# Performance work log

Measured on AMD Instinct MI355X. Metric: run time of the kernel, lower is better.

## Reference

```python
import jax, jax.numpy as jnp
import numpy as np

B, N, D = 2, 8192, 128
TEMP_MIN = 1e-4


def setup_inputs() -> dict:
    key = jax.random.key(0)
    k0, k1 = jax.random.split(key)
    feats0 = jax.random.normal(k0, (B, N, D), dtype=jnp.float32)
    feats1 = jax.random.normal(k1, (B, N, D), dtype=jnp.float32)
    temp = jnp.ones((), dtype=jnp.float32)  # nn.Parameter(temp_init=1.0)
    return {"feats0": feats0, "feats1": feats1, "temp": temp}


def reference(feats0, feats1, temp):
    x2 = jnp.sum(feats0 * feats0, axis=-1, keepdims=True)            # [B, N0, 1]
    y2 = jnp.sum(feats1 * feats1, axis=-1, keepdims=True)            # [B, N1, 1]
    dists = x2 - 2.0 * jnp.einsum('bnd,bmd->bnm', feats0, feats1)
    dists = dists + jnp.swapaxes(y2, -2, -1)                          # [B, N0, N1]

    t = jnp.maximum(temp * temp, TEMP_MIN)                            # get_temp()
    probs = jax.nn.softmax(-dists / t, axis=-1)                       # [B, N0, N1]

    idx = jnp.argmax(probs, axis=-1)                                  # [B, N0]
    asgn = jax.nn.one_hot(idx, probs.shape[-1], dtype=probs.dtype)    # hard one-hot
    # straight-through: value = one-hot, gradient = softmax gradient
    asgn_diff = asgn - jax.lax.stop_gradient(probs) + probs
    return asgn_diff, idx
```

## Files before the change

kernel.cpp:

```cpp
#include <hip/hip_runtime.h>
#include <hip/hip_fp16.h>
#include <cstdint>
#include <cstddef>

#define NPTS 8192
#define DDIM 128
#define BATCH 2
#define NROWS (BATCH * NPTS)
#define EPSGAP 1.0f
#define NCOLT 64
#define WCAP 512

typedef __attribute__((ext_vector_type(8))) _Float16 half8v;
typedef __attribute__((ext_vector_type(4))) float f32x4;

typedef __attribute__((address_space(3))) unsigned int as3_uint;
typedef const __attribute__((address_space(1))) unsigned int as1_uint;

__global__ void split_kernel(const float* __restrict__ f0, const float* __restrict__ f1,
                             unsigned short* __restrict__ Aext, unsigned short* __restrict__ Bext,
                             float* __restrict__ y2) {
    const unsigned half = gridDim.x >> 1;
    const bool isB = blockIdx.x >= half;
    const float* src = isB ? f1 : f0;
    unsigned short* dst = isB ? Bext : Aext;
    size_t t = (size_t)(blockIdx.x - (isB ? half : 0)) * 256 + threadIdx.x;
    size_t row = t >> 5;
    int kc = (int)(t & 31) * 4;
    float4 v = reinterpret_cast<const float4*>(src)[t];
    ushort4 h;
    h.x = __half_as_ushort(__float2half(v.x));
    h.y = __half_as_ushort(__float2half(v.y));
    h.z = __half_as_ushort(__float2half(v.z));
    h.w = __half_as_ushort(__float2half(v.w));
    *reinterpret_cast<ushort4*>(&dst[row * 128 + kc]) = h;

    if (isB) {
        float s = fmaf(v.x, v.x, fmaf(v.y, v.y, fmaf(v.z, v.z, v.w * v.w)));
#pragma unroll
        for (int off = 16; off >= 1; off >>= 1) s += __shfl_xor(s, off);
        if ((t & 31) == 0) y2[row] = s;
    }
}

__global__ __launch_bounds__(256) void gemm_mfma(
    const unsigned short* __restrict__ Aext,
    const unsigned short* __restrict__ Bext,
    const float* __restrict__ y2g,
    float* __restrict__ pv1, float* __restrict__ pv2, unsigned int* __restrict__ pidx,
    float* __restrict__ outZero)
{
    __shared__ __align__(16) short As[128 * 64];
    __shared__ __align__(16) short Bs[128 * 64];
    __shared__ float rv1[2][128];
    __shared__ float rv2[2][128];
    __shared__ unsigned int ri[2][128];

    const unsigned flat = blockIdx.x;
    const unsigned wg   = (flat & 7u) * 1024u + (flat >> 3);
    const int bm  = wg & 63;
    const int bnc = (int)((wg >> 6) & 63);
    const int b   = (int)(wg >> 12);

    const int tid  = threadIdx.x;
    const int lane = tid & 63;
    const int wid  = tid >> 6;
    const int wr   = wid >> 1, wc = wid & 1;
    const int l15  = lane & 15, l4 = lane >> 4;
    const int row0 = bm * 128, col0 = bnc * 128;

    const unsigned short* Abase = Aext + ((size_t)b * NPTS + row0) * 128;
    const unsigned short* Bbase = Bext + ((size_t)b * NPTS + col0) * 128;

    f32x4 acc[4][4];
#pragma unroll
    for (int i = 0; i < 4; ++i)
#pragma unroll
        for (int j = 0; j < 4; ++j) acc[i][j] = (f32x4)0.0f;

#pragma unroll
    for (int kk = 0; kk < 2; ++kk) {
        __syncthreads();
        {
            const int ko = kk * 64;
#pragma unroll
            for (int it = 0; it < 4; ++it) {
                int flat2 = it * 256 + tid;
                int r = flat2 >> 3, kc = flat2 & 7;
                int kcs = kc ^ (r & 7);
                const unsigned short* ga = Abase + (size_t)r * 128 + ko + kcs * 8;
                const unsigned short* gb = Bbase + (size_t)r * 128 + ko + kcs * 8;
                __builtin_amdgcn_global_load_lds((as1_uint*)ga, (as3_uint*)&As[flat2 * 8], 16, 0, 0);
                __builtin_amdgcn_global_load_lds((as1_uint*)gb, (as3_uint*)&Bs[flat2 * 8], 16, 0, 0);
            }
        }
        __syncthreads();
#pragma unroll
        for (int ks = 0; ks < 2; ++ks) {
            half8v a[4], bf[4];
#pragma unroll
            for (int i = 0; i < 4; ++i) {
                int ra = wr * 64 + i * 16 + l15;
                int ch = ks * 4 + l4;
                a[i] = *reinterpret_cast<const half8v*>(&As[ra * 64 + ((ch ^ (ra & 7)) << 3)]);
            }
#pragma unroll
            for (int j = 0; j < 4; ++j) {
                int rb = wc * 64 + j * 16 + l15;
                int ch = ks * 4 + l4;
                bf[j] = *reinterpret_cast<const half8v*>(&Bs[rb * 64 + ((ch ^ (rb & 7)) << 3)]);
            }
#pragma unroll
            for (int i = 0; i < 4; ++i)
#pragma unroll
                for (int j = 0; j < 4; ++j)
                    acc[i][j] = __builtin_amdgcn_mfma_f32_16x16x32_f16(a[i], bf[j], acc[i][j], 0, 0, 0);
        }
    }

    const float* y2b = y2g + b * NPTS;
    float yv[4];
#pragma unroll
    for (int j = 0; j < 4; ++j) yv[j] = y2b[col0 + wc * 64 + j * 16 + l15];

    {
        f32x4* o4 = reinterpret_cast<f32x4*>(outZero) + (size_t)wg * 4096;
        const f32x4 z = (f32x4)0.0f;
#pragma unroll
        for (int it = 0; it < 16; ++it)
            __builtin_nontemporal_store(z, &o4[it * 256 + tid]);
    }

#pragma unroll
    for (int i = 0; i < 4; ++i) {
#pragma unroll
        for (int q = 0; q < 4; ++q) {
            float v1 = INFINITY, v2 = INFINITY;
            unsigned int mi = 0u;
#pragma unroll
            for (int j = 0; j < 4; ++j) {
                const float v = fmaf(-2.0f, acc[i][j][q], yv[j]);
                const unsigned int m = (unsigned)(col0 + wc * 64 + j * 16 + l15);
                if (v < v1) { v2 = v1; v1 = v; mi = m; }
                else        { v2 = fminf(v2, v); }
            }
#pragma unroll
            for (int off = 1; off < 16; off <<= 1) {
                float o1 = __shfl_xor(v1, off);
                float o2 = __shfl_xor(v2, off);
                unsigned int oi = __shfl_xor(mi, off);
                if (o1 < v1 || (o1 == v1 && oi < mi)) { v2 = fminf(v1, o2); v1 = o1; mi = oi; }
                else                                  { v2 = fminf(v2, fminf(o1, o2)); }
            }
            if (l15 == 0) {
                const int rl = wr * 64 + i * 16 + l4 * 4 + q;
                rv1[wc][rl] = v1; rv2[wc][rl] = v2; ri[wc][rl] = mi;
            }
        }
    }
    __syncthreads();
    if (tid < 128) {
        float a1 = rv1[0][tid], a2 = rv2[0][tid];
        unsigned int ai = ri[0][tid];
        const float o1 = rv1[1][tid], o2 = rv2[1][tid];
        const unsigned int oi = ri[1][tid];
        if (o1 < a1 || (o1 == a1 && oi < ai)) { a2 = fminf(a1, o2); a1 = o1; ai = oi; }
        else                                  { a2 = fminf(a2, fminf(o1, o2)); }
        const size_t gr = (size_t)b * NPTS + row0 + tid;
        pv1[(size_t)bnc * NROWS + gr] = a1;
        pv2[(size_t)bnc * NROWS + gr] = a2;
        pidx[(size_t)bnc * NROWS + gr] = ai;
    }
}

__global__ __launch_bounds__(256) void finalize_kernel(
    const float* __restrict__ f0, const float* __restrict__ f1,
    const float* __restrict__ pv1, const float* __restrict__ pv2,
    const unsigned int* __restrict__ pidx,
    float* __restrict__ out)
{
    __shared__ float xrow[4][DDIM];
    __shared__ unsigned int cand[4][WCAP];
    __shared__ int ncand[4];
    __shared__ float s_best[64];
    __shared__ unsigned char s_flag[64];
    __shared__ int s_nflag;

    const int tid = threadIdx.x;
    const int gr0 = blockIdx.x * 64;

    if (tid == 0) s_nflag = 0;
    __syncthreads();

    {
        const int r  = tid >> 2;
        const int q  = tid & 3;
        const int gr = gr0 + r;
        float a1 = INFINITY, a2 = INFINITY;
        unsigned int ai = 0u;
#pragma unroll 4
        for (int c = 0; c < 16; ++c) {
            const int cs = q * 16 + c;
            const size_t base = (size_t)cs * NROWS + gr;
            const float o1 = pv1[base];
            const float o2 = pv2[base];
            const unsigned int oi = pidx[base];
            if (o1 < a1 || (o1 == a1 && oi < ai)) { a2 = fminf(a1, o2); a1 = o1; ai = oi; }
            else                                  { a2 = fminf(a2, fminf(o1, o2)); }
        }
#pragma unroll
        for (int off = 1; off < 4; off <<= 1) {
            const float o1 = __shfl_xor(a1, off);
            const float o2 = __shfl_xor(a2, off);
            const unsigned int oi = __shfl_xor(ai, off);
            if (o1 < a1 || (o1 == a1 && oi < ai)) { a2 = fminf(a1, o2); a1 = o1; ai = oi; }
            else                                  { a2 = fminf(a2, fminf(o1, o2)); }
        }
        if (q == 0) {
            if (a2 - a1 < EPSGAP) {
                const int p = atomicAdd(&s_nflag, 1);
                s_flag[p] = (unsigned char)r;
                s_best[r] = a1;
            } else {
                out[(size_t)gr * NPTS + ai] = 1.0f;
                out[(size_t)BATCH * NPTS * NPTS + gr] = (float)ai;
            }
        }
    }
    __syncthreads();

    const int nf   = s_nflag;
    const int w    = tid >> 6;
    const int lane = tid & 63;

    for (int li = w; li < nf; li += 4) {
        const int rr = (int)s_flag[li];
        const int gr = gr0 + rr;
        const int b = gr >> 13, n = gr & (NPTS - 1);
        const float W = s_best[rr] + EPSGAP;

        if (lane == 0) ncand[w] = 0;
        const float* xp = f0 + ((size_t)b * NPTS + n) * DDIM;
        xrow[w][lane]      = xp[lane];
        xrow[w][lane + 64] = xp[lane + 64];

        {
            const size_t base = (size_t)lane * NROWS + gr;
            const float t1 = pv1[base];
            if (t1 <= W) {
                if (pv2[base] <= W) {
                    int p = atomicAdd(&ncand[w], 128);
                    if (p + 128 <= WCAP)
                        for (int c = 0; c < 128; ++c) cand[w][p + c] = (unsigned)(lane * 128 + c);
                } else {
                    int p = atomicAdd(&ncand[w], 1);
                    if (p < WCAP) cand[w][p] = pidx[base];
                }
            }
        }
        asm volatile("s_waitcnt lgkmcnt(0)" ::: "memory");

        const int nc = ncand[w];
        double bv = 1e300;
        unsigned int bi = 0xFFFFFFFFu;
        const float4* xpv = reinterpret_cast<const float4*>(xrow[w]);
        if (nc <= WCAP) {
            for (int c = lane; c < nc; c += 64) {
                const unsigned int m = cand[w][c];
                const float4* ypv = reinterpret_cast<const float4*>(f1 + ((size_t)b * NPTS + m) * DDIM);
                double s0 = 0.0, s1 = 0.0, s2 = 0.0, s3 = 0.0;
#pragma unroll 8
                for (int k4 = 0; k4 < DDIM / 4; ++k4) {
                    const float4 y = ypv[k4];
                    const float4 x = xpv[k4];
                    s0 = fma((double)y.x, (double)y.x - 2.0 * (double)x.x, s0);
                    s1 = fma((double)y.y, (double)y.y - 2.0 * (double)x.y, s1);
                    s2 = fma((double)y.z, (double)y.z - 2.0 * (double)x.z, s2);
                    s3 = fma((double)y.w, (double)y.w - 2.0 * (double)x.w, s3);
                }
                const double v = (s0 + s1) + (s2 + s3);
                if (v < bv || (v == bv && m < bi)) { bv = v; bi = m; }
            }
        } else {
            for (int m = lane; m < NPTS; m += 64) {
                const float4* ypv = reinterpret_cast<const float4*>(f1 + ((size_t)b * NPTS + m) * DDIM);
                double s0 = 0.0, s1 = 0.0, s2 = 0.0, s3 = 0.0;
#pragma unroll 4
                for (int k4 = 0; k4 < DDIM / 4; ++k4) {
                    const float4 y = ypv[k4];
                    const float4 x = xpv[k4];
                    s0 = fma((double)y.x, (double)y.x - 2.0 * (double)x.x, s0);
                    s1 = fma((double)y.y, (double)y.y - 2.0 * (double)x.y, s1);
                    s2 = fma((double)y.z, (double)y.z - 2.0 * (double)x.z, s2);
                    s3 = fma((double)y.w, (double)y.w - 2.0 * (double)x.w, s3);
                }
                const double v = (s0 + s1) + (s2 + s3);
                if (v < bv || (v == bv && (unsigned)m < bi)) { bv = v; bi = (unsigned)m; }
            }
        }
#pragma unroll
        for (int off = 1; off < 64; off <<= 1) {
            const double ov = __shfl_xor(bv, off);
            const unsigned int oi = __shfl_xor(bi, off);
            if (ov < bv || (ov == bv && oi < bi)) { bv = ov; bi = oi; }
        }
        if (lane == 0) {
            out[(size_t)gr * NPTS + bi] = 1.0f;
            out[(size_t)BATCH * NPTS * NPTS + gr] = (float)bi;
        }
        asm volatile("s_waitcnt lgkmcnt(0)" ::: "memory");
    }
}

extern "C" void kernel_launch(void* const* d_in, const int* in_sizes, int n_in,
                              void* d_out, int out_size, void* d_ws, size_t ws_size,
                              hipStream_t stream)
{
    const float* f0 = (const float*)d_in[0];
    const float* f1 = (const float*)d_in[1];
    float* out = (float*)d_out;

    char* wsb = (char*)d_ws;
    unsigned short* Aext = (unsigned short*)wsb;                  wsb += (size_t)BATCH * NPTS * 128 * 2;
    unsigned short* Bext = (unsigned short*)wsb;                  wsb += (size_t)BATCH * NPTS * 128 * 2;
    float* y2            = (float*)wsb;                           wsb += (size_t)NROWS * 4;
    float* pv1           = (float*)wsb;                           wsb += (size_t)NCOLT * NROWS * 4;
    float* pv2           = (float*)wsb;                           wsb += (size_t)NCOLT * NROWS * 4;
    unsigned int* pidx   = (unsigned int*)wsb;

    split_kernel<<<2 * (BATCH * NPTS * 32) / 256, 256, 0, stream>>>(f0, f1, Aext, Bext, y2);
    gemm_mfma<<<NPTS / 128 * NPTS / 128 * BATCH, 256, 0, stream>>>(Aext, Bext, y2, pv1, pv2, pidx, out);
    finalize_kernel<<<NROWS / 64, 256, 0, stream>>>(f0, f1, pv1, pv2, pidx, out);
}
```

Baseline: 193.5 us.

## Fuse fp16 conversion and column norms into GEMM, drop split kernel

Removes the separate split kernel that converted features to fp16 and computed y2. The GEMM now loads fp32 tiles straight into LDS in four 32-wide phases and converts to fp16 in registers with cvt_pkrtz. It also accumulates the B-row squared norms from the same LDS reads and reduces them through shared memory. The block-to-XCD mapping is changed as well. This saves a launch and the intermediate global round trip, at the cost of twice the global and LDS traffic per tile, more barriers, and round-toward-zero conversion.

```diff
diff --git a/kernel.cpp b/kernel.cpp
--- a/kernel.cpp
+++ b/kernel.cpp
@@ -17,50 +17,33 @@
 typedef __attribute__((address_space(3))) unsigned int as3_uint;
 typedef const __attribute__((address_space(1))) unsigned int as1_uint;
 
-__global__ void split_kernel(const float* __restrict__ f0, const float* __restrict__ f1,
-                             unsigned short* __restrict__ Aext, unsigned short* __restrict__ Bext,
-                             float* __restrict__ y2) {
-    const unsigned half = gridDim.x >> 1;
-    const bool isB = blockIdx.x >= half;
-    const float* src = isB ? f1 : f0;
-    unsigned short* dst = isB ? Bext : Aext;
-    size_t t = (size_t)(blockIdx.x - (isB ? half : 0)) * 256 + threadIdx.x;
-    size_t row = t >> 5;
-    int kc = (int)(t & 31) * 4;
-    float4 v = reinterpret_cast<const float4*>(src)[t];
-    ushort4 h;
-    h.x = __half_as_ushort(__float2half(v.x));
-    h.y = __half_as_ushort(__float2half(v.y));
-    h.z = __half_as_ushort(__float2half(v.z));
-    h.w = __half_as_ushort(__float2half(v.w));
-    *reinterpret_cast<ushort4*>(&dst[row * 128 + kc]) = h;
-
-    if (isB) {
-        float s = fmaf(v.x, v.x, fmaf(v.y, v.y, fmaf(v.z, v.z, v.w * v.w)));
-#pragma unroll
-        for (int off = 16; off >= 1; off >>= 1) s += __shfl_xor(s, off);
-        if ((t & 31) == 0) y2[row] = s;
-    }
+static __device__ __forceinline__ half8v cvt8(f32x4 lo, f32x4 hi) {
+    union { unsigned int u[4]; half8v h; } cv;
+    cv.u[0] = __builtin_bit_cast(unsigned int, __builtin_amdgcn_cvt_pkrtz(lo.x, lo.y));
+    cv.u[1] = __builtin_bit_cast(unsigned int, __builtin_amdgcn_cvt_pkrtz(lo.z, lo.w));
+    cv.u[2] = __builtin_bit_cast(unsigned int, __builtin_amdgcn_cvt_pkrtz(hi.x, hi.y));
+    cv.u[3] = __builtin_bit_cast(unsigned int, __builtin_amdgcn_cvt_pkrtz(hi.z, hi.w));
+    return cv.h;
 }
 
 __global__ __launch_bounds__(256) void gemm_mfma(
-    const unsigned short* __restrict__ Aext,
-    const unsigned short* __restrict__ Bext,
-    const float* __restrict__ y2g,
+    const float* __restrict__ f0, const float* __restrict__ f1,
     float* __restrict__ pv1, float* __restrict__ pv2, unsigned int* __restrict__ pidx,
     float* __restrict__ outZero)
 {
-    __shared__ __align__(16) short As[128 * 64];
-    __shared__ __align__(16) short Bs[128 * 64];
+    __shared__ __align__(16) float As[128 * 32];
+    __shared__ __align__(16) float Bs[128 * 32];
     __shared__ float rv1[2][128];
     __shared__ float rv2[2][128];
     __shared__ unsigned int ri[2][128];
+    __shared__ float y2s[128];
 
     const unsigned flat = blockIdx.x;
-    const unsigned wg   = (flat & 7u) * 1024u + (flat >> 3);
-    const int bm  = wg & 63;
-    const int bnc = (int)((wg >> 6) & 63);
-    const int b   = (int)(wg >> 12);
+    const unsigned xcd  = flat & 7u;
+    const unsigned q    = flat >> 3;
+    const int b    = (int)(xcd >> 2);
+    const int bm   = (int)(((xcd >> 1) & 1u) * 32 + (q & 31));
+    const int bnc  = (int)((xcd & 1u) * 32 + (q >> 5));
 
     const int tid  = threadIdx.x;
     const int lane = tid & 63;
@@ -69,8 +52,8 @@
     const int l15  = lane & 15, l4 = lane >> 4;
     const int row0 = bm * 128, col0 = bnc * 128;
 
-    const unsigned short* Abase = Aext + ((size_t)b * NPTS + row0) * 128;
-    const unsigned short* Bbase = Bext + ((size_t)b * NPTS + col0) * 128;
+    const float* Abase = f0 + ((size_t)b * NPTS + row0) * DDIM;
+    const float* Bbase = f1 + ((size_t)b * NPTS + col0) * DDIM;
 
     f32x4 acc[4][4];
 #pragma unroll
@@ -78,53 +61,68 @@
 #pragma unroll
         for (int j = 0; j < 4; ++j) acc[i][j] = (f32x4)0.0f;
 
-#pragma unroll
-    for (int kk = 0; kk < 2; ++kk) {
+    float y2p[4] = {0.0f, 0.0f, 0.0f, 0.0f};
+
+#pragma unroll
+    for (int ph = 0; ph < 4; ++ph) {
         __syncthreads();
         {
-            const int ko = kk * 64;
+            const int ko = ph * 32;
 #pragma unroll
             for (int it = 0; it < 4; ++it) {
                 int flat2 = it * 256 + tid;
                 int r = flat2 >> 3, kc = flat2 & 7;
                 int kcs = kc ^ (r & 7);
-                const unsigned short* ga = Abase + (size_t)r * 128 + ko + kcs * 8;
-                const unsigned short* gb = Bbase + (size_t)r * 128 + ko + kcs * 8;
-                __builtin_amdgcn_global_load_lds((as1_uint*)ga, (as3_uint*)&As[flat2 * 8], 16, 0, 0);
-                __builtin_amdgcn_global_load_lds((as1_uint*)gb, (as3_uint*)&Bs[flat2 * 8], 16, 0, 0);
+                const float* ga = Abase + (size_t)r * DDIM + ko + kcs * 4;
+                const float* gb = Bbase + (size_t)r * DDIM + ko + kcs * 4;
+                __builtin_amdgcn_global_load_lds((as1_uint*)ga, (as3_uint*)&As[flat2 * 4], 16, 0, 0);
+                __builtin_amdgcn_global_load_lds((as1_uint*)gb, (as3_uint*)&Bs[flat2 * 4], 16, 0, 0);
             }
         }
         __syncthreads();
-#pragma unroll
-        for (int ks = 0; ks < 2; ++ks) {
-            half8v a[4], bf[4];
-#pragma unroll
-            for (int i = 0; i < 4; ++i) {
-                int ra = wr * 64 + i * 16 + l15;
-                int ch = ks * 4 + l4;
-                a[i] = *reinterpret_cast<const half8v*>(&As[ra * 64 + ((ch ^ (ra & 7)) << 3)]);
-            }
-#pragma unroll
-            for (int j = 0; j < 4; ++j) {
-                int rb = wc * 64 + j * 16 + l15;
-                int ch = ks * 4 + l4;
-                bf[j] = *reinterpret_cast<const half8v*>(&Bs[rb * 64 + ((ch ^ (rb & 7)) << 3)]);
-            }
-#pragma unroll
-            for (int i = 0; i < 4; ++i)
-#pragma unroll
-                for (int j = 0; j < 4; ++j)
-                    acc[i][j] = __builtin_amdgcn_mfma_f32_16x16x32_f16(a[i], bf[j], acc[i][j], 0, 0, 0);
-        }
-    }
-
-    const float* y2b = y2g + b * NPTS;
+        half8v a[4], bf[4];
+#pragma unroll
+        for (int i = 0; i < 4; ++i) {
+            const int ra = wr * 64 + i * 16 + l15;
+            const int c0 = (2 * l4) ^ (ra & 7);
+            const int c1 = (2 * l4 + 1) ^ (ra & 7);
+            const f32x4 lo = *reinterpret_cast<const f32x4*>(&As[ra * 32 + c0 * 4]);
+            const f32x4 hi = *reinterpret_cast<const f32x4*>(&As[ra * 32 + c1 * 4]);
+            a[i] = cvt8(lo, hi);
+        }
+#pragma unroll
+        for (int j = 0; j < 4; ++j) {
+            const int rb = wc * 64 + j * 16 + l15;
+            const int c0 = (2 * l4) ^ (rb & 7);
+            const int c1 = (2 * l4 + 1) ^ (rb & 7);
+            const f32x4 lo = *reinterpret_cast<const f32x4*>(&Bs[rb * 32 + c0 * 4]);
+            const f32x4 hi = *reinterpret_cast<const f32x4*>(&Bs[rb * 32 + c1 * 4]);
+            y2p[j] = fmaf(lo.x, lo.x, fmaf(lo.y, lo.y, fmaf(lo.z, lo.z, fmaf(lo.w, lo.w,
+                     fmaf(hi.x, hi.x, fmaf(hi.y, hi.y, fmaf(hi.z, hi.z, fmaf(hi.w, hi.w, y2p[j]))))))));
+            bf[j] = cvt8(lo, hi);
+        }
+#pragma unroll
+        for (int i = 0; i < 4; ++i)
+#pragma unroll
+            for (int j = 0; j < 4; ++j)
+                acc[i][j] = __builtin_amdgcn_mfma_f32_16x16x32_f16(a[i], bf[j], acc[i][j], 0, 0, 0);
+    }
+
+#pragma unroll
+    for (int j = 0; j < 4; ++j) {
+        float s = y2p[j];
+        s += __shfl_xor(s, 16);
+        s += __shfl_xor(s, 32);
+        if (wr == 0 && l4 == 0) y2s[wc * 64 + j * 16 + l15] = s;
+    }
+    __syncthreads();
+
     float yv[4];
 #pragma unroll
-    for (int j = 0; j < 4; ++j) yv[j] = y2b[col0 + wc * 64 + j * 16 + l15];
+    for (int j = 0; j < 4; ++j) yv[j] = y2s[wc * 64 + j * 16 + l15];
 
     {
-        f32x4* o4 = reinterpret_cast<f32x4*>(outZero) + (size_t)wg * 4096;
+        f32x4* o4 = reinterpret_cast<f32x4*>(outZero) + (size_t)flat * 4096;
         const f32x4 z = (f32x4)0.0f;
 #pragma unroll
         for (int it = 0; it < 16; ++it)
@@ -134,12 +132,12 @@
 #pragma unroll
     for (int i = 0; i < 4; ++i) {
 #pragma unroll
-        for (int q = 0; q < 4; ++q) {
+        for (int q2 = 0; q2 < 4; ++q2) {
             float v1 = INFINITY, v2 = INFINITY;
             unsigned int mi = 0u;
 #pragma unroll
             for (int j = 0; j < 4; ++j) {
-                const float v = fmaf(-2.0f, acc[i][j][q], yv[j]);
+                const float v = fmaf(-2.0f, acc[i][j][q2], yv[j]);
                 const unsigned int m = (unsigned)(col0 + wc * 64 + j * 16 + l15);
                 if (v < v1) { v2 = v1; v1 = v; mi = m; }
                 else        { v2 = fminf(v2, v); }
@@ -153,7 +151,7 @@
                 else                                  { v2 = fminf(v2, fminf(o1, o2)); }
             }
             if (l15 == 0) {
-                const int rl = wr * 64 + i * 16 + l4 * 4 + q;
+                const int rl = wr * 64 + i * 16 + l4 * 4 + q2;
                 rv1[wc][rl] = v1; rv2[wc][rl] = v2; ri[wc][rl] = mi;
             }
         }
@@ -321,14 +319,10 @@
     float* out = (float*)d_out;
 
     char* wsb = (char*)d_ws;
-    unsigned short* Aext = (unsigned short*)wsb;                  wsb += (size_t)BATCH * NPTS * 128 * 2;
-    unsigned short* Bext = (unsigned short*)wsb;                  wsb += (size_t)BATCH * NPTS * 128 * 2;
-    float* y2            = (float*)wsb;                           wsb += (size_t)NROWS * 4;
     float* pv1           = (float*)wsb;                           wsb += (size_t)NCOLT * NROWS * 4;
     float* pv2           = (float*)wsb;                           wsb += (size_t)NCOLT * NROWS * 4;
     unsigned int* pidx   = (unsigned int*)wsb;
 
-    split_kernel<<<2 * (BATCH * NPTS * 32) / 256, 256, 0, stream>>>(f0, f1, Aext, Bext, y2);
-    gemm_mfma<<<NPTS / 128 * NPTS / 128 * BATCH, 256, 0, stream>>>(Aext, Bext, y2, pv1, pv2, pidx, out);
+    gemm_mfma<<<NPTS / 128 * NPTS / 128 * BATCH, 256, 0, stream>>>(f0, f1, pv1, pv2, pidx, out);
     finalize_kernel<<<NROWS / 64, 256, 0, stream>>>(f0, f1, pv1, pv2, pidx, out);
 }
```

New measurement: 221.9 us. +14.6%, slower.
